# Performance work log

Measured on AMD Instinct MI355X. Metric: run time of the kernel, lower is better.

## Reference

```python
import jax, jax.numpy as jnp
import numpy as np

B, CIN, COUT, H, W_SP = 16, 128, 128, 56, 56
E, KH, KW = 4, 3, 3

def setup_inputs() -> dict:
    key = jax.random.key(0)
    k1, k2, k3 = jax.random.split(key, 3)
    x = jax.random.normal(k1, (B, CIN, H, W_SP), dtype=jnp.float32)
    routing_weights = jax.random.uniform(k2, (B, E), dtype=jnp.float32)
    # expert conv kernels, OIHW, stacked over experts: [E, COUT, CIN, KH, KW]
    W = jax.random.normal(k3, (E, COUT, CIN, KH, KW), dtype=jnp.float32) * 0.05
    return {"x": x, "routing_weights": routing_weights, "W": W}

def reference(x, routing_weights, W):
    # Each expert: full Conv2d(stride=1, padding=1, dilation=1, groups=1, no bias)
    def one_expert(w):  # w: [COUT, CIN, KH, KW]
        return jax.lax.conv_general_dilated(
            x, w,
            window_strides=(1, 1),
            padding=((1, 1), (1, 1)),
            dimension_numbers=("NCHW", "OIHW", "NCHW"),
        )
    expert_outs = jax.vmap(one_expert)(W)  # [E, B, COUT, H, W]
    # per-sample scalar mix: sum_e routing[b, e] * expert_outs[e, b]
    out = jnp.einsum("ebchw,be->bchw", expert_outs, routing_weights)
    return out
```

## Files before the change

kernel.cpp:

```cpp
#include <hip/hip_runtime.h>


typedef float  f32x16 __attribute__((ext_vector_type(16)));
typedef short  s16x8  __attribute__((ext_vector_type(8)));
typedef unsigned short u16;

#define CIN   128
#define COUT  128
#define HH    56
#define WW    56
#define SP    (HH*WW)
#define EW    147456
#define BW_   147456
#define XSTR  72
#define XB    (4*66*XSTR)
#define AB    8192

static __device__ __forceinline__ u16 f2bf(float f) {
    unsigned u = __builtin_bit_cast(unsigned, f);
    return (u16)((u + 0x7FFFu + ((u >> 16) & 1u)) >> 16);
}

static __device__ __forceinline__ void gload16(const void* g, void* l) {
    __builtin_amdgcn_global_load_lds(
        (const __attribute__((address_space(1))) void*)g,
        (__attribute__((address_space(3))) void*)l, 16, 0, 0);
}

__global__ __launch_bounds__(256) void mix_kernel(const float* __restrict__ W,
                                                  const float* __restrict__ r,
                                                  u16* __restrict__ Wmix) {
    int o = blockIdx.x * 256 + threadIdx.x;
    int ci_l = o & 31;
    int o2   = o >> 5;
    int co   = o2 & 127;
    int o3   = o2 >> 7;
    int tap  = o3 % 9;
    int cc   = o3 / 9;
    size_t src = ((size_t)co * CIN + cc*32 + ci_l) * 9 + tap;
    float w0 = W[src], w1 = W[src + EW], w2 = W[src + 2*EW], w3 = W[src + 3*EW];
    #pragma unroll
    for (int b = 0; b < 16; ++b) {
        float acc = r[b*4+0]*w0 + r[b*4+1]*w1 + r[b*4+2]*w2 + r[b*4+3]*w3;
        Wmix[(size_t)b * BW_ + o] = f2bf(acc);
    }
}

__global__ __launch_bounds__(512, 4) void conv_mfma(const float* __restrict__ x,
                                                    const u16* __restrict__ Wmix,
                                                    float* __restrict__ out) {
    __shared__ __align__(16) char ldsb[XB + 4*AB];

    const int bid = blockIdx.x;
    const int bs  = (bid & 7) * 56 + (bid >> 3);
    const int b   = bs / 28;
    const int ph  = bs % 28;
    const int t    = threadIdx.x;
    const int lane = t & 63;
    const int wid  = t >> 6;
    const int wm   = (wid >> 2) & 1;
    const int wn   = (wid >> 1) & 1;
    const int wp   = wid & 1;
    const int l31  = lane & 31;
    const int khalf= lane >> 5;

    const u16*   WmixB = Wmix + (size_t)b * BW_;
    const float* xbB   = x + (size_t)b * CIN * SP;

    const int ssl = (t & 3) ^ ((t >> 3) & 3);

    f32x16 acc[2];
    acc[0] = (f32x16)0.f;
    acc[1] = (f32x16)0.f;

    auto stageA = [&](int it) {
        char* ldst = ldsb + XB + (it & 3) * AB + wid * 1024;
        const u16* ga = WmixB + it * 4096 + (t >> 2) * 32 + ssl * 8;
        gload16(ga, ldst);
    };

    auto stageX = [&](int cc) {
        #pragma unroll
        for (int i = 0; i < 2; ++i) {
            int slot = i * 512 + t;
            int c    = 1 + (slot & 63);
            int row  = (slot >> 6) & 3;
            int g    = slot >> 8;
            int rr   = 2*ph - 1 + row;
            int w    = c - 1;
            bool ok  = ((unsigned)rr < 56u) && (w < 56);
            const float* p = xbB + (size_t)(cc*32 + g*8) * SP + rr*56 + w;
            s16x8 v;
            #pragma unroll
            for (int j = 0; j < 8; ++j) {
                float f = ok ? p[(size_t)j * SP] : 0.f;
                v[j] = (short)f2bf(f);
            }
            *(s16x8*)(ldsb + (row*66 + c)*XSTR + g*16) = v;
        }
    };

    auto compute = [&](int it, int kh, int kw) {
        const char* Ab = ldsb + XB + (it & 3) * AB;
        #pragma unroll
        for (int ksub = 0; ksub < 2; ++ksub) {
            const int s = ksub * 2 + khalf;
            s16x8 af[2], bv;
            #pragma unroll
            for (int mf = 0; mf < 2; ++mf)
                af[mf] = *(const s16x8*)(Ab + (wm*64 + mf*32 + l31)*64
                                            + ((s ^ ((l31 >> 1) & 3)) * 16));
            const int c = wp*32 + l31 + kw;
            bv = *(const s16x8*)(ldsb + ((wn + kh)*66 + c)*XSTR + s*16);
            #pragma unroll
            for (int mf = 0; mf < 2; ++mf)
                acc[mf] = __builtin_amdgcn_mfma_f32_32x32x16_bf16(
                    af[mf], bv, acc[mf], 0, 0, 0);
        }
    };

    if (t < 32) {
        int row = t >> 3, col = ((t >> 2) & 1) ? 65 : 0, sl = t & 3;
        *(s16x8*)(ldsb + (row*66 + col)*XSTR + sl*16) = (s16x8)0;
    }
    stageA(0);
    stageA(1);
    stageX(0);
    asm volatile("s_waitcnt lgkmcnt(0)" ::: "memory");
    __builtin_amdgcn_sched_barrier(0);
    __builtin_amdgcn_s_barrier();
    __builtin_amdgcn_sched_barrier(0);

    #pragma unroll
    for (int cc = 0; cc < 4; ++cc) {
        if (cc) {
            __builtin_amdgcn_sched_barrier(0);
            __builtin_amdgcn_s_barrier();
            __builtin_amdgcn_sched_barrier(0);
            stageX(cc);
            asm volatile("s_waitcnt lgkmcnt(0)" ::: "memory");
            __builtin_amdgcn_sched_barrier(0);
            __builtin_amdgcn_s_barrier();
            __builtin_amdgcn_sched_barrier(0);
        }
        #pragma unroll
        for (int tap = 0; tap < 9; ++tap) {
            const int it = cc * 9 + tap;
            if (it + 2 < 36) {
                stageA(it + 2);
                asm volatile("s_waitcnt vmcnt(2)" ::: "memory");
            } else if (it + 1 < 36) {
                asm volatile("s_waitcnt vmcnt(1)" ::: "memory");
            } else {
                asm volatile("s_waitcnt vmcnt(0)" ::: "memory");
            }
            __builtin_amdgcn_s_barrier();
            __builtin_amdgcn_sched_barrier(0);
            __builtin_amdgcn_s_setprio(1);
            compute(it, tap / 3, tap % 3);
            __builtin_amdgcn_s_setprio(0);
        }
    }

    const int w = wp * 32 + l31;
    if (w < 56) {
        const int hrow = 2 * ph + wn;
        #pragma unroll
        for (int mf = 0; mf < 2; ++mf) {
            #pragma unroll
            for (int rg = 0; rg < 16; ++rg) {
                int co = wm*64 + mf*32 + (rg & 3) + 8*(rg >> 2) + 4*khalf;
                out[(((size_t)b*COUT + co)*HH + hrow)*WW + w] = acc[mf][rg];
            }
        }
    }
}

extern "C" void kernel_launch(void* const* d_in, const int* in_sizes, int n_in,
                              void* d_out, int out_size, void* d_ws, size_t ws_size,
                              hipStream_t stream) {
    const float* x = (const float*)d_in[0];
    const float* r = (const float*)d_in[1];
    const float* W = (const float*)d_in[2];
    float* outp = (float*)d_out;
    u16* Wmix = (u16*)d_ws;

    mix_kernel<<<576, 256, 0, stream>>>(W, r, Wmix);
    conv_mfma <<<448, 512, 0, stream>>>(x, Wmix, outp);
}
```

Before: 34.47 us.

## Double-buffer input tile in LDS and prefetch next channel chunk into registers

The x tile in LDS gets two buffers. The next 32-channel chunk's global loads are issued into registers at tap 6 of the current chunk, then converted to bf16 and written to the alternate buffer. This removes the two block-wide barriers around each input restage and hides the x load latency behind MFMA work. The cost is doubled LDS for x, which may lower occupancy, plus 16 extra live float registers and hand-tuned vmcnt counts that must stay in step with the in-flight loads.

```diff
diff --git a/kernel.cpp b/kernel.cpp
--- a/kernel.cpp
+++ b/kernel.cpp
@@ -49,7 +49,7 @@
 __global__ __launch_bounds__(512, 4) void conv_mfma(const float* __restrict__ x,
                                                     const u16* __restrict__ Wmix,
                                                     float* __restrict__ out) {
-    __shared__ __align__(16) char ldsb[XB + 4*AB];
+    __shared__ __align__(16) char ldsb[2*XB + 4*AB];
 
     const int bid = blockIdx.x;
     const int bs  = (bid & 7) * 56 + (bid >> 3);
@@ -69,39 +69,54 @@
 
     const int ssl = (t & 3) ^ ((t >> 3) & 3);
 
+    bool  xok[2];
+    const float* xsp[2];
+    int   xdst[2];
+    #pragma unroll
+    for (int i = 0; i < 2; ++i) {
+        int slot = i * 512 + t;
+        int c    = 1 + (slot & 63);
+        int row  = (slot >> 6) & 3;
+        int g    = slot >> 8;
+        int rr   = 2*ph - 1 + row;
+        int w    = c - 1;
+        xok[i]   = ((unsigned)rr < 56u) && (w < 56);
+        xsp[i]   = xok[i] ? (xbB + (size_t)(g*8) * SP + rr*56 + w) : xbB;
+        xdst[i]  = (row*66 + c)*XSTR + g*16;
+    }
+    float xr[2][8];
+
+    auto issueX = [&](int cc) {
+        #pragma unroll
+        for (int i = 0; i < 2; ++i) {
+            const float* p = xok[i] ? (xsp[i] + (size_t)cc*32*SP) : xbB;
+            #pragma unroll
+            for (int j = 0; j < 8; ++j) xr[i][j] = p[(size_t)j * SP];
+        }
+    };
+    auto writeX = [&](int cc) {
+        #pragma unroll
+        for (int i = 0; i < 2; ++i) {
+            s16x8 v;
+            #pragma unroll
+            for (int j = 0; j < 8; ++j)
+                v[j] = xok[i] ? (short)f2bf(xr[i][j]) : (short)0;
+            *(s16x8*)(ldsb + (cc & 1)*XB + xdst[i]) = v;
+        }
+    };
+
+    auto stageA = [&](int it) {
+        char* ldst = ldsb + 2*XB + (it & 3) * AB + wid * 1024;
+        const u16* ga = WmixB + it * 4096 + (t >> 2) * 32 + ssl * 8;
+        gload16(ga, ldst);
+    };
+
     f32x16 acc[2];
     acc[0] = (f32x16)0.f;
     acc[1] = (f32x16)0.f;
 
-    auto stageA = [&](int it) {
-        char* ldst = ldsb + XB + (it & 3) * AB + wid * 1024;
-        const u16* ga = WmixB + it * 4096 + (t >> 2) * 32 + ssl * 8;
-        gload16(ga, ldst);
-    };
-
-    auto stageX = [&](int cc) {
-        #pragma unroll
-        for (int i = 0; i < 2; ++i) {
-            int slot = i * 512 + t;
-            int c    = 1 + (slot & 63);
-            int row  = (slot >> 6) & 3;
-            int g    = slot >> 8;
-            int rr   = 2*ph - 1 + row;
-            int w    = c - 1;
-            bool ok  = ((unsigned)rr < 56u) && (w < 56);
-            const float* p = xbB + (size_t)(cc*32 + g*8) * SP + rr*56 + w;
-            s16x8 v;
-            #pragma unroll
-            for (int j = 0; j < 8; ++j) {
-                float f = ok ? p[(size_t)j * SP] : 0.f;
-                v[j] = (short)f2bf(f);
-            }
-            *(s16x8*)(ldsb + (row*66 + c)*XSTR + g*16) = v;
-        }
-    };
-
-    auto compute = [&](int it, int kh, int kw) {
-        const char* Ab = ldsb + XB + (it & 3) * AB;
+    auto compute = [&](int it, int kh, int kw, int xbase) {
+        const char* Ab = ldsb + 2*XB + (it & 3) * AB;
         #pragma unroll
         for (int ksub = 0; ksub < 2; ++ksub) {
             const int s = ksub * 2 + khalf;
@@ -111,7 +126,7 @@
                 af[mf] = *(const s16x8*)(Ab + (wm*64 + mf*32 + l31)*64
                                             + ((s ^ ((l31 >> 1) & 3)) * 16));
             const int c = wp*32 + l31 + kw;
-            bv = *(const s16x8*)(ldsb + ((wn + kh)*66 + c)*XSTR + s*16);
+            bv = *(const s16x8*)(ldsb + xbase + ((wn + kh)*66 + c)*XSTR + s*16);
             #pragma unroll
             for (int mf = 0; mf < 2; ++mf)
                 acc[mf] = __builtin_amdgcn_mfma_f32_32x32x16_bf16(
@@ -119,45 +134,50 @@
         }
     };
 
-    if (t < 32) {
-        int row = t >> 3, col = ((t >> 2) & 1) ? 65 : 0, sl = t & 3;
-        *(s16x8*)(ldsb + (row*66 + col)*XSTR + sl*16) = (s16x8)0;
-    }
+    if (t < 64) {
+        int bufi = (t >> 5) & 1, row = (t >> 3) & 3;
+        int col = ((t >> 2) & 1) ? 65 : 0, sl = t & 3;
+        *(s16x8*)(ldsb + bufi*XB + (row*66 + col)*XSTR + sl*16) = (s16x8)0;
+    }
+    issueX(0);
+    __builtin_amdgcn_sched_barrier(0);
     stageA(0);
     stageA(1);
-    stageX(0);
+    __builtin_amdgcn_sched_barrier(0);
+    asm volatile("s_waitcnt vmcnt(2)" ::: "memory");
+    writeX(0);
     asm volatile("s_waitcnt lgkmcnt(0)" ::: "memory");
-    __builtin_amdgcn_sched_barrier(0);
-    __builtin_amdgcn_s_barrier();
     __builtin_amdgcn_sched_barrier(0);
 
     #pragma unroll
     for (int cc = 0; cc < 4; ++cc) {
         if (cc) {
-            __builtin_amdgcn_sched_barrier(0);
-            __builtin_amdgcn_s_barrier();
-            __builtin_amdgcn_sched_barrier(0);
-            stageX(cc);
+            asm volatile("s_waitcnt vmcnt(2)" ::: "memory");
+            writeX(cc);
             asm volatile("s_waitcnt lgkmcnt(0)" ::: "memory");
             __builtin_amdgcn_sched_barrier(0);
-            __builtin_amdgcn_s_barrier();
-            __builtin_amdgcn_sched_barrier(0);
         }
         #pragma unroll
         for (int tap = 0; tap < 9; ++tap) {
             const int it = cc * 9 + tap;
-            if (it + 2 < 36) {
-                stageA(it + 2);
-                asm volatile("s_waitcnt vmcnt(2)" ::: "memory");
-            } else if (it + 1 < 36) {
-                asm volatile("s_waitcnt vmcnt(1)" ::: "memory");
+            if (it + 2 < 36) stageA(it + 2);
+            if (tap == 6 && cc < 3) {
+                __builtin_amdgcn_sched_barrier(0);
+                issueX(cc + 1);
+            }
+            __builtin_amdgcn_sched_barrier(0);
+            if (cc < 3) {
+                if (tap <= 6) asm volatile("s_waitcnt vmcnt(2)" ::: "memory");
+                else          asm volatile("s_waitcnt vmcnt(18)" ::: "memory");
             } else {
-                asm volatile("s_waitcnt vmcnt(0)" ::: "memory");
+                if      (tap <= 6) asm volatile("s_waitcnt vmcnt(2)" ::: "memory");
+                else if (tap == 7) asm volatile("s_waitcnt vmcnt(1)" ::: "memory");
+                else               asm volatile("s_waitcnt vmcnt(0)" ::: "memory");
             }
             __builtin_amdgcn_s_barrier();
             __builtin_amdgcn_sched_barrier(0);
             __builtin_amdgcn_s_setprio(1);
-            compute(it, tap / 3, tap % 3);
+            compute(it, tap / 3, tap % 3, (cc & 1) * XB);
             __builtin_amdgcn_s_setprio(0);
         }
     }
```

Result: no change. 34.54 us (+0.2%).

## Split K across wave pairs with 2x2 MFMA tiles and LDS reduction

Applied to the files above, without the earlier changes.

Reassigns the eight waves so each computes a 64x64 output tile (2x2 MFMA fragments) over half of the 32-channel K slice, instead of a 64x32 tile over the full slice. Each wave now loads 2 A and 2 B fragments for 4 MFMAs rather than 4 A and 2 B for 4, which cuts LDS fragment reads per MFMA. The two K halves are summed at the end through LDS, reusing the A staging buffers, before the stores. This costs twice the accumulator registers, an extra reduction phase with barriers, and leaves half the waves idle during the output write.

```diff
diff --git a/kernel.cpp b/kernel.cpp
--- a/kernel.cpp
+++ b/kernel.cpp
@@ -2,6 +2,7 @@
 
 
 typedef float  f32x16 __attribute__((ext_vector_type(16)));
+typedef float  f32x4  __attribute__((ext_vector_type(4)));
 typedef short  s16x8  __attribute__((ext_vector_type(8)));
 typedef unsigned short u16;
 
@@ -58,20 +59,23 @@
     const int t    = threadIdx.x;
     const int lane = t & 63;
     const int wid  = t >> 6;
-    const int wm   = (wid >> 2) & 1;
-    const int wn   = (wid >> 1) & 1;
-    const int wp   = wid & 1;
+    const int wk   = wid >> 2;
+    const int wm   = (wid >> 1) & 1;
+    const int wr   = wid & 1;
     const int l31  = lane & 31;
     const int khalf= lane >> 5;
+    const int s16i = wk * 2 + khalf;
 
     const u16*   WmixB = Wmix + (size_t)b * BW_;
     const float* xbB   = x + (size_t)b * CIN * SP;
 
     const int ssl = (t & 3) ^ ((t >> 3) & 3);
 
-    f32x16 acc[2];
-    acc[0] = (f32x16)0.f;
-    acc[1] = (f32x16)0.f;
+    f32x16 acc[2][2];
+    #pragma unroll
+    for (int mf = 0; mf < 2; ++mf)
+        #pragma unroll
+        for (int nf = 0; nf < 2; ++nf) acc[mf][nf] = (f32x16)0.f;
 
     auto stageA = [&](int it) {
         char* ldst = ldsb + XB + (it & 3) * AB + wid * 1024;
@@ -102,21 +106,22 @@
 
     auto compute = [&](int it, int kh, int kw) {
         const char* Ab = ldsb + XB + (it & 3) * AB;
-        #pragma unroll
-        for (int ksub = 0; ksub < 2; ++ksub) {
-            const int s = ksub * 2 + khalf;
-            s16x8 af[2], bv;
-            #pragma unroll
-            for (int mf = 0; mf < 2; ++mf)
-                af[mf] = *(const s16x8*)(Ab + (wm*64 + mf*32 + l31)*64
-                                            + ((s ^ ((l31 >> 1) & 3)) * 16));
-            const int c = wp*32 + l31 + kw;
-            bv = *(const s16x8*)(ldsb + ((wn + kh)*66 + c)*XSTR + s*16);
-            #pragma unroll
-            for (int mf = 0; mf < 2; ++mf)
-                acc[mf] = __builtin_amdgcn_mfma_f32_32x32x16_bf16(
-                    af[mf], bv, acc[mf], 0, 0, 0);
-        }
+        s16x8 af[2], bv[2];
+        #pragma unroll
+        for (int mf = 0; mf < 2; ++mf)
+            af[mf] = *(const s16x8*)(Ab + (wm*64 + mf*32 + l31)*64
+                                        + ((s16i ^ ((l31 >> 1) & 3)) * 16));
+        #pragma unroll
+        for (int nf = 0; nf < 2; ++nf) {
+            const int c = nf*32 + l31 + kw;
+            bv[nf] = *(const s16x8*)(ldsb + ((wr + kh)*66 + c)*XSTR + s16i*16);
+        }
+        #pragma unroll
+        for (int mf = 0; mf < 2; ++mf)
+            #pragma unroll
+            for (int nf = 0; nf < 2; ++nf)
+                acc[mf][nf] = __builtin_amdgcn_mfma_f32_32x32x16_bf16(
+                    af[mf], bv[nf], acc[mf][nf], 0, 0, 0);
     };
 
     if (t < 32) {
@@ -162,15 +167,51 @@
         }
     }
 
-    const int w = wp * 32 + l31;
-    if (w < 56) {
-        const int hrow = 2 * ph + wn;
-        #pragma unroll
-        for (int mf = 0; mf < 2; ++mf) {
-            #pragma unroll
-            for (int rg = 0; rg < 16; ++rg) {
-                int co = wm*64 + mf*32 + (rg & 3) + 8*(rg >> 2) + 4*khalf;
-                out[(((size_t)b*COUT + co)*HH + hrow)*WW + w] = acc[mf][rg];
+    __builtin_amdgcn_s_barrier();
+    const int idx = wm*2 + wr;
+    #pragma unroll
+    for (int mf = 0; mf < 2; ++mf) {
+        if (wk == 1) {
+            #pragma unroll
+            for (int nf = 0; nf < 2; ++nf)
+                #pragma unroll
+                for (int q = 0; q < 4; ++q) {
+                    f32x4 v;
+                    #pragma unroll
+                    for (int j = 0; j < 4; ++j) v[j] = acc[mf][nf][q*4 + j];
+                    *(f32x4*)(ldsb + XB + idx*8192 + (nf*4 + q)*1024 + lane*16) = v;
+                }
+        }
+        asm volatile("s_waitcnt lgkmcnt(0)" ::: "memory");
+        __builtin_amdgcn_s_barrier();
+        if (wk == 0) {
+            #pragma unroll
+            for (int nf = 0; nf < 2; ++nf)
+                #pragma unroll
+                for (int q = 0; q < 4; ++q) {
+                    f32x4 v = *(const f32x4*)(ldsb + XB + idx*8192
+                                              + (nf*4 + q)*1024 + lane*16);
+                    #pragma unroll
+                    for (int j = 0; j < 4; ++j) acc[mf][nf][q*4 + j] += v[j];
+                }
+        }
+        if (mf == 0) __builtin_amdgcn_s_barrier();
+    }
+
+    if (wk == 0) {
+        const int hrow = 2 * ph + wr;
+        #pragma unroll
+        for (int nf = 0; nf < 2; ++nf) {
+            const int w = nf * 32 + l31;
+            if (w < 56) {
+                #pragma unroll
+                for (int mf = 0; mf < 2; ++mf) {
+                    #pragma unroll
+                    for (int rg = 0; rg < 16; ++rg) {
+                        int co = wm*64 + mf*32 + (rg & 3) + 8*(rg >> 2) + 4*khalf;
+                        out[(((size_t)b*COUT + co)*HH + hrow)*WW + w] = acc[mf][nf][rg];
+                    }
+                }
             }
         }
     }
```

Measured after the change: 35.27 us. 2.3% more time.

## Double-buffer MFMA operand fragments in registers and drop a barrier per channel chunk

Applied to the files above, without the earlier changes.

LDS reads of the A and B fragments for the next K-step now happen right after the step's barrier, into a second register buffer, so the current step's MFMAs overlap the next step's LDS latency. The barrier before restaging the X tile for each new channel chunk is removed; the per-tap barrier is relied on instead, and the vmcnt waits are adjusted to match. The cost is extra VGPRs for the operand buffers, plus a risk of LDS read/write ordering hazards from the removed barrier.

```diff
diff --git a/kernel.cpp b/kernel.cpp
--- a/kernel.cpp
+++ b/kernel.cpp
@@ -73,6 +73,8 @@
     acc[0] = (f32x16)0.f;
     acc[1] = (f32x16)0.f;
 
+    s16x8 frg[2][6];
+
     auto stageA = [&](int it) {
         char* ldst = ldsb + XB + (it & 3) * AB + wid * 1024;
         const u16* ga = WmixB + it * 4096 + (t >> 2) * 32 + ssl * 8;
@@ -100,23 +102,36 @@
         }
     };
 
-    auto compute = [&](int it, int kh, int kw) {
-        const char* Ab = ldsb + XB + (it & 3) * AB;
+    auto readA = [&](int n, int buf) {
+        const char* Ab = ldsb + XB + (n & 3) * AB;
         #pragma unroll
         for (int ksub = 0; ksub < 2; ++ksub) {
             const int s = ksub * 2 + khalf;
-            s16x8 af[2], bv;
             #pragma unroll
             for (int mf = 0; mf < 2; ++mf)
-                af[mf] = *(const s16x8*)(Ab + (wm*64 + mf*32 + l31)*64
-                                            + ((s ^ ((l31 >> 1) & 3)) * 16));
+                frg[buf][ksub*2 + mf] = *(const s16x8*)(
+                    Ab + (wm*64 + mf*32 + l31)*64 + ((s ^ ((l31 >> 1) & 3)) * 16));
+        }
+    };
+    auto readB = [&](int n, int buf) {
+        const int tap = n % 9;
+        const int kh  = tap / 3;
+        const int kw  = tap % 3;
+        #pragma unroll
+        for (int ksub = 0; ksub < 2; ++ksub) {
+            const int s = ksub * 2 + khalf;
             const int c = wp*32 + l31 + kw;
-            bv = *(const s16x8*)(ldsb + ((wn + kh)*66 + c)*XSTR + s*16);
+            frg[buf][4 + ksub] = *(const s16x8*)(
+                ldsb + ((wn + kh)*66 + c)*XSTR + s*16);
+        }
+    };
+    auto mfmas = [&](int buf) {
+        #pragma unroll
+        for (int ksub = 0; ksub < 2; ++ksub)
             #pragma unroll
             for (int mf = 0; mf < 2; ++mf)
                 acc[mf] = __builtin_amdgcn_mfma_f32_32x32x16_bf16(
-                    af[mf], bv, acc[mf], 0, 0, 0);
-        }
+                    frg[buf][ksub*2 + mf], frg[buf][4 + ksub], acc[mf], 0, 0, 0);
     };
 
     if (t < 32) {
@@ -130,34 +145,36 @@
     __builtin_amdgcn_sched_barrier(0);
     __builtin_amdgcn_s_barrier();
     __builtin_amdgcn_sched_barrier(0);
+    readA(0, 0);
+    readB(0, 0);
 
     #pragma unroll
     for (int cc = 0; cc < 4; ++cc) {
         if (cc) {
-            __builtin_amdgcn_sched_barrier(0);
-            __builtin_amdgcn_s_barrier();
-            __builtin_amdgcn_sched_barrier(0);
             stageX(cc);
             asm volatile("s_waitcnt lgkmcnt(0)" ::: "memory");
             __builtin_amdgcn_sched_barrier(0);
+        }
+        #pragma unroll
+        for (int tap = 0; tap < 9; ++tap) {
+            const int n   = cc * 9 + tap;
+            const int cur = n & 1;
+            if (n + 2 < 36) {
+                stageA(n + 2);
+                asm volatile("s_waitcnt vmcnt(1)" ::: "memory");
+            } else if (n + 1 < 36) {
+                asm volatile("s_waitcnt vmcnt(0)" ::: "memory");
+            }
             __builtin_amdgcn_s_barrier();
             __builtin_amdgcn_sched_barrier(0);
-        }
-        #pragma unroll
-        for (int tap = 0; tap < 9; ++tap) {
-            const int it = cc * 9 + tap;
-            if (it + 2 < 36) {
-                stageA(it + 2);
-                asm volatile("s_waitcnt vmcnt(2)" ::: "memory");
-            } else if (it + 1 < 36) {
-                asm volatile("s_waitcnt vmcnt(1)" ::: "memory");
-            } else {
-                asm volatile("s_waitcnt vmcnt(0)" ::: "memory");
-            }
-            __builtin_amdgcn_s_barrier();
+            if (n + 1 < 36) {
+                readA(n + 1, cur ^ 1);
+                if (tap != 8) readB(n + 1, cur ^ 1);
+            }
+            if (tap == 0 && cc) readB(n, cur);
             __builtin_amdgcn_sched_barrier(0);
             __builtin_amdgcn_s_setprio(1);
-            compute(it, tap / 3, tap % 3);
+            mfmas(cur);
             __builtin_amdgcn_s_setprio(0);
         }
     }
```

New measurement: 34.52 us. About the same (+0.2%).
